# Kernel tuning notes

Hardware: AMD Instinct MI355X
Metric: run time of the kernel (lower is better)

Reference implementation:

```python
import jax, jax.numpy as jnp
import numpy as np

B, C, H, W = 4, 16, 256, 256
O = 32
KH = KW = 3
PAD = 1


def setup_inputs() -> dict:
    key = jax.random.key(0)
    ks = jax.random.split(key, 6)
    d_in = C * KH * KW          # 144
    d_out = O * KH * KW         # 288
    s1 = 1.0 / np.sqrt(d_in)
    s2 = 1.0 / np.sqrt(O)
    return {
        "x": jax.random.normal(ks[0], (B, C, H, W), dtype=jnp.float32),
        "W1": jax.random.uniform(ks[1], (O, d_in), jnp.float32, -s1, s1),
        "b1": jax.random.uniform(ks[2], (O,), jnp.float32, -s1, s1),
        "W2": jax.random.uniform(ks[3], (d_out, O), jnp.float32, -s2, s2),
        "b2": jax.random.uniform(ks[4], (d_out,), jnp.float32, -s2, s2),
        "bias": jax.random.uniform(ks[5], (O,), jnp.float32, -s1, s1),
    }


def _unfold(x):
    """im2col matching torch F.unfold ordering (c, kh, kw): -> [B, H*W, C*KH*KW]."""
    b, c, h, w = x.shape
    xp = jnp.pad(x, ((0, 0), (0, 0), (PAD, PAD), (PAD, PAD)))
    # stack the KH*KW shifted views: [B, C, KH*KW, H, W]
    shifts = [xp[:, :, i:i + h, j:j + w] for i in range(KH) for j in range(KW)]
    p = jnp.stack(shifts, axis=2)
    # -> [B, H, W, C, KH*KW] -> [B, L, C*KH*KW]  (c-major, then (i,j))
    p = p.transpose(0, 3, 4, 1, 2)
    return p.reshape(b, h * w, c * KH * KW)


def reference(x, W1, b1, W2, b2, bias):
    b, c, h, w = x.shape
    L = h * w
    feat = _unfold(x)                                   # [B, L, C*9]
    # per-pixel kernel generator MLP
    hid = jnp.tanh(jnp.einsum('blf,of->blo', feat, W1) + b1)          # [B, L, O]
    kern = jnp.einsum('blo,go->blg', hid, W2) + b2                    # [B, L, O*9]
    kern = kern.reshape(b, L, O, KH * KW)                             # [B, L, O, 9]
    # contract per-pixel kernel with its patch (channels summed):
    # out[b,l,o] = sum_{c,i,j} K[b,l,o,ij] * P[b,l,c,ij]
    patch_c = feat.reshape(b, L, c, KH * KW).sum(axis=2)              # [B, L, 9]
    out = jnp.einsum('blok,blk->blo', kern, patch_c)                  # [B, L, O]
    out = out.transpose(0, 2, 1).reshape(b, O, h, w)
    return out + bias[None, :, None, None]
```

## Files before the change

### kernel.cpp

```cpp
#include <hip/hip_runtime.h>

#define CC 16
#define OO 32
#define LL 65536

typedef __attribute__((ext_vector_type(8))) short bf16x8;
typedef __attribute__((ext_vector_type(4))) float f32x4;
typedef __attribute__((ext_vector_type(4))) int   i32x4;

static __device__ __forceinline__ ushort f2b(float f) {
    union { float f; unsigned u; } v; v.f = f;
    return (ushort)((v.u + 0x7fff + ((v.u >> 16) & 1)) >> 16);
}
static __device__ __forceinline__ unsigned pk2(float fl, float fh) {
    unsigned ul = __float_as_uint(fl) + 0x8000u;
    unsigned uh = __float_as_uint(fh) + 0x8000u;
    return __builtin_amdgcn_perm(uh, ul, 0x07060302);
}

__global__ void prepass(const float* __restrict__ W1, const float* __restrict__ b1,
                        const float* __restrict__ W2, const float* __restrict__ b2,
                        const float* __restrict__ bias,
                        ushort* __restrict__ w1f, ushort* __restrict__ w2f) {
    int idx = blockIdx.x * 256 + threadIdx.x;
    if (idx < 5120) {
        int f = idx >> 9, lane = (idx >> 3) & 63, j = idx & 7;
        int ks = f >> 1, ot = f & 1, lm = lane & 15, g = lane >> 4;
        int o = ot * 16 + lm, kk = ks * 32 + g * 8 + j;
        int r = kk >> 4, c = kk & 15;
        float v = (kk < 144) ? W1[o * 144 + c * 9 + r] : (kk == 144 ? b1[o] : 0.f);
        w1f[idx] = f2b(v);
    } else if (idx < 15360) {
        int i2 = idx - 5120;
        int f = i2 >> 9, lane = (i2 >> 3) & 63, j = i2 & 7;
        int ks = f >> 1, ot = f & 1, lm = lane & 15, g = lane >> 4;
        int o = ot * 16 + lm, kk = ks * 32 + g * 8 + j;
        float v;
        if      (kk < 288) v = W2[o * 288 + kk];
        else if (kk < 297) v = b2[o * 9 + (kk - 288)];
        else if (kk == 297) v = bias[o];
        else               v = 0.f;
        w2f[i2] = f2b(v);
    }
}

__global__ __launch_bounds__(256, 2) void dynaconv_mfma(
    const float* __restrict__ x, const ushort* __restrict__ w1f,
    const ushort* __restrict__ w2f, float* __restrict__ out)
{
    __shared__ __align__(16) ushort xs[4][260][24];
    __shared__ __align__(16) float  S[4][260];
    __shared__ __align__(16) float  hidT[4][16][36];

    const int tid  = threadIdx.x;
    const int wv   = tid >> 6;
    const int lane = tid & 63;
    const int g    = lane >> 4;
    const int lm   = lane & 15;

    const int vbid = (blockIdx.x & 7) * 64 + (blockIdx.x >> 3);
    const int b    = vbid >> 7;
    const int h0   = (vbid & 127) * 2;

    bf16x8 W1R[10], W2R[20];
#pragma unroll
    for (int f = 0; f < 10; ++f) W1R[f] = *(const bf16x8*)(w1f + (f * 64 + lane) * 8);
#pragma unroll
    for (int f = 0; f < 20; ++f) W2R[f] = *(const bf16x8*)(w2f + (f * 64 + lane) * 8);

    const float* xb = x + b * (CC * LL);
    {
        int offr[4]; bool okr[4];
#pragma unroll
        for (int r = 0; r < 4; ++r) {
            const int hh = h0 - 1 + r;
            okr[r] = (unsigned)hh < 256u;
            offr[r] = (okr[r] ? hh : 0) * 256 + tid;
        }
        float sr[4] = {0.f, 0.f, 0.f, 0.f};
#pragma unroll
        for (int cp = 0; cp < 8; ++cp) {
            const float* p0 = xb + (2 * cp) * LL;
            const float* p1 = p0 + LL;
#pragma unroll
            for (int r = 0; r < 4; ++r) {
                float va = p0[offr[r]], vb = p1[offr[r]];
                va = okr[r] ? va : 0.f; vb = okr[r] ? vb : 0.f;
                sr[r] += va + vb;
                *(unsigned*)&xs[r][tid + 1][2 * cp] = pk2(va, vb);
            }
        }
#pragma unroll
        for (int r = 0; r < 4; ++r) S[r][tid + 1] = sr[r];
        if (tid < 128) { int r = tid >> 5, side = (tid >> 4) & 1, c = tid & 15; xs[r][side * 257][c] = 0; }
        if (tid < 8)   S[tid >> 1][(tid & 1) * 257] = 0.f;
    }
    __syncthreads();

    int soff[5];
#pragma unroll
    for (int ks = 0; ks < 5; ++ks) {
        int r = 2 * ks + (g >> 1); if (r > 8) r = 8;
        int r3 = (r * 11) >> 5, rm = r - 3 * r3;
        soff[ks] = (r3 * 260 + rm + lm) * 24 + (g & 1) * 8;
    }
    const ushort* xsf = &xs[0][0][0];

    for (int hr = 0; hr < 2; ++hr) {
        const int hb = hr * (260 * 24);
#pragma unroll
        for (int t = 0; t < 4; ++t) {
            const int w0t = wv * 64 + t * 16;
            const int tb = w0t * 24 + hb;

            f32x4 a1[2] = {{0.f,0.f,0.f,0.f},{0.f,0.f,0.f,0.f}};
#pragma unroll
            for (int ks = 0; ks < 5; ++ks) {
                bf16x8 ff = *(const bf16x8*)(xsf + soff[ks] + tb);
                if (ks == 4) {
                    i32x4 wd = *(i32x4*)&ff;
                    wd[0] = (g < 2) ? wd[0] : (g == 2 ? 0x3F80 : 0);
                    wd[1] = (g < 2) ? wd[1] : 0;
                    wd[2] = (g < 2) ? wd[2] : 0;
                    wd[3] = (g < 2) ? wd[3] : 0;
                    ff = *(bf16x8*)&wd;
                }
                a1[0] = __builtin_amdgcn_mfma_f32_16x16x32_bf16(W1R[2 * ks],     ff, a1[0], 0, 0, 0);
                a1[1] = __builtin_amdgcn_mfma_f32_16x16x32_bf16(W1R[2 * ks + 1], ff, a1[1], 0, 0, 0);
            }

#pragma unroll
            for (int ot = 0; ot < 2; ++ot)
#pragma unroll
                for (int q = 0; q < 4; ++q) {
                    float e = __expf(2.f * a1[ot][q]);
                    hidT[wv][lm][ot * 16 + g * 4 + q] = 1.f - 2.f / (e + 1.f);
                }
            f32x4 h0v = *(const f32x4*)&hidT[wv][lm][g * 8];
            f32x4 h1v = *(const f32x4*)&hidT[wv][lm][g * 8 + 4];

            float pcv[9];
#pragma unroll
            for (int r = 0; r < 9; ++r) pcv[r] = S[r / 3 + hr][w0t + lm + (r % 3)];

            f32x4 a2[2] = {{0.f,0.f,0.f,0.f},{0.f,0.f,0.f,0.f}};
#pragma unroll
            for (int ks = 0; ks < 9; ++ks) {
                const float p = pcv[ks];
                i32x4 wd;
                wd[0] = (int)pk2(h0v[0] * p, h0v[1] * p);
                wd[1] = (int)pk2(h0v[2] * p, h0v[3] * p);
                wd[2] = (int)pk2(h1v[0] * p, h1v[1] * p);
                wd[3] = (int)pk2(h1v[2] * p, h1v[3] * p);
                bf16x8 ff2 = *(bf16x8*)&wd;
                a2[0] = __builtin_amdgcn_mfma_f32_16x16x32_bf16(W2R[2 * ks],     ff2, a2[0], 0, 0, 0);
                a2[1] = __builtin_amdgcn_mfma_f32_16x16x32_bf16(W2R[2 * ks + 1], ff2, a2[1], 0, 0, 0);
            }
            {
                i32x4 wd;
                wd[0] = (g == 0) ? (int)pk2(pcv[0], pcv[1]) : ((g == 1) ? (int)pk2(pcv[8], 1.f) : 0);
                wd[1] = (g == 0) ? (int)pk2(pcv[2], pcv[3]) : 0;
                wd[2] = (g == 0) ? (int)pk2(pcv[4], pcv[5]) : 0;
                wd[3] = (g == 0) ? (int)pk2(pcv[6], pcv[7]) : 0;
                bf16x8 ff2 = *(bf16x8*)&wd;
                a2[0] = __builtin_amdgcn_mfma_f32_16x16x32_bf16(W2R[18], ff2, a2[0], 0, 0, 0);
                a2[1] = __builtin_amdgcn_mfma_f32_16x16x32_bf16(W2R[19], ff2, a2[1], 0, 0, 0);
            }

            float* ob = out + b * (OO * LL) + (h0 + hr) * 256 + w0t + lm;
#pragma unroll
            for (int ot = 0; ot < 2; ++ot)
#pragma unroll
                for (int q = 0; q < 4; ++q)
                    __builtin_nontemporal_store(a2[ot][q], &ob[(ot * 16 + g * 4 + q) * LL]);
        }
    }
}

extern "C" void kernel_launch(void* const* d_in, const int* in_sizes, int n_in,
                              void* d_out, int out_size, void* d_ws, size_t ws_size,
                              hipStream_t stream) {
    const float* x    = (const float*)d_in[0];
    const float* W1   = (const float*)d_in[1];
    const float* b1   = (const float*)d_in[2];
    const float* W2   = (const float*)d_in[3];
    const float* b2   = (const float*)d_in[4];
    const float* bias = (const float*)d_in[5];
    float* out = (float*)d_out;

    ushort* w1f = (ushort*)d_ws;
    ushort* w2f = w1f + 5120;

    prepass<<<60, 256, 0, stream>>>(W1, b1, W2, b2, bias, w1f, w2f);
    dynaconv_mfma<<<512, 256, 0, stream>>>(x, w1f, w2f, out);
}
```

Before: 26.83 us.

## Use 512-thread blocks, stage W2 in LDS, and replace hidT LDS transpose with shuffles

Doubles the block to 512 threads, so each wave handles one output row and two 16-pixel tiles per iteration. W2 fragments move from registers into shared memory to lower register pressure for higher occupancy. The LDS round-trip used to transpose hidden activations is replaced by packed bf16 cross-lane shuffles. The x tile is shrunk to 16 channels with no padding, and the bias-one column now comes from a small LDS buffer. Output stores become regular rather than nontemporal. The costs are added LDS traffic for W2 on every MFMA and possible bank conflicts from the unpadded layout.

```diff
diff --git a/kernel.cpp b/kernel.cpp
--- a/kernel.cpp
+++ b/kernel.cpp
@@ -16,6 +16,10 @@
     unsigned ul = __float_as_uint(fl) + 0x8000u;
     unsigned uh = __float_as_uint(fh) + 0x8000u;
     return __builtin_amdgcn_perm(uh, ul, 0x07060302);
+}
+static __device__ __forceinline__ float tanh_fast(float x) {
+    float e = __expf(2.f * x);
+    return 1.f - 2.f / (e + 1.f);
 }
 
 __global__ void prepass(const float* __restrict__ W1, const float* __restrict__ b1,
@@ -44,13 +48,14 @@
     }
 }
 
-__global__ __launch_bounds__(256, 2) void dynaconv_mfma(
+__global__ __launch_bounds__(512, 4) void dynaconv_mfma(
     const float* __restrict__ x, const ushort* __restrict__ w1f,
     const ushort* __restrict__ w2f, float* __restrict__ out)
 {
-    __shared__ __align__(16) ushort xs[4][260][24];
-    __shared__ __align__(16) float  S[4][260];
-    __shared__ __align__(16) float  hidT[4][16][36];
+    __shared__ __align__(16) ushort xs[4][258][16];
+    __shared__ __align__(16) float  S[4][258];
+    __shared__ __align__(16) ushort extb[16];
+    __shared__ __align__(16) ushort W2L[20 * 512];
 
     const int tid  = threadIdx.x;
     const int wv   = tid >> 6;
@@ -62,39 +67,50 @@
     const int b    = vbid >> 7;
     const int h0   = (vbid & 127) * 2;
 
-    bf16x8 W1R[10], W2R[20];
+    bf16x8 W1R[10];
 #pragma unroll
     for (int f = 0; f < 10; ++f) W1R[f] = *(const bf16x8*)(w1f + (f * 64 + lane) * 8);
-#pragma unroll
-    for (int f = 0; f < 20; ++f) W2R[f] = *(const bf16x8*)(w2f + (f * 64 + lane) * 8);
+
+    {
+        const i32x4* src = (const i32x4*)w2f;
+        i32x4*       dst = (i32x4*)W2L;
+#pragma unroll
+        for (int k = 0; k < 3; ++k) {
+            int i = tid + k * 512;
+            if (i < 1280) dst[i] = src[i];
+        }
+    }
 
     const float* xb = x + b * (CC * LL);
     {
-        int offr[4]; bool okr[4];
-#pragma unroll
-        for (int r = 0; r < 4; ++r) {
-            const int hh = h0 - 1 + r;
-            okr[r] = (unsigned)hh < 256u;
-            offr[r] = (okr[r] ? hh : 0) * 256 + tid;
-        }
-        float sr[4] = {0.f, 0.f, 0.f, 0.f};
+        const int col = tid & 255;
+        const int rp  = tid >> 8;
+        const int ra  = rp * 2;
+        const int ha  = h0 - 1 + ra;
+        const int hbb = ha + 1;
+        const bool oka = (unsigned)ha  < 256u;
+        const bool okb = (unsigned)hbb < 256u;
+        const int offa = (oka ? ha  : 0) * 256 + col;
+        const int offb = (okb ? hbb : 0) * 256 + col;
+        float sa = 0.f, sb = 0.f;
 #pragma unroll
         for (int cp = 0; cp < 8; ++cp) {
             const float* p0 = xb + (2 * cp) * LL;
             const float* p1 = p0 + LL;
-#pragma unroll
-            for (int r = 0; r < 4; ++r) {
-                float va = p0[offr[r]], vb = p1[offr[r]];
-                va = okr[r] ? va : 0.f; vb = okr[r] ? vb : 0.f;
-                sr[r] += va + vb;
-                *(unsigned*)&xs[r][tid + 1][2 * cp] = pk2(va, vb);
-            }
-        }
-#pragma unroll
-        for (int r = 0; r < 4; ++r) S[r][tid + 1] = sr[r];
-        if (tid < 128) { int r = tid >> 5, side = (tid >> 4) & 1, c = tid & 15; xs[r][side * 257][c] = 0; }
-        if (tid < 8)   S[tid >> 1][(tid & 1) * 257] = 0.f;
-    }
+            float va0 = p0[offa], vb0 = p1[offa];
+            float va1 = p0[offb], vb1 = p1[offb];
+            va0 = oka ? va0 : 0.f; vb0 = oka ? vb0 : 0.f;
+            va1 = okb ? va1 : 0.f; vb1 = okb ? vb1 : 0.f;
+            sa += va0 + vb0; sb += va1 + vb1;
+            *(unsigned*)&xs[ra][col + 1][2 * cp]     = pk2(va0, vb0);
+            *(unsigned*)&xs[ra + 1][col + 1][2 * cp] = pk2(va1, vb1);
+        }
+        S[ra][col + 1] = sa; S[ra + 1][col + 1] = sb;
+    }
+    if (tid < 64) { int r = tid >> 4, side = (tid >> 3) & 1, cw = tid & 7;
+                    *(unsigned*)&xs[r][side * 257][2 * cw] = 0u; }
+    if (tid < 8)  S[tid >> 1][(tid & 1) * 257] = 0.f;
+    if (tid < 16) extb[tid] = (tid == 0) ? (ushort)0x3F80 : (ushort)0;
     __syncthreads();
 
     int soff[5];
@@ -102,77 +118,121 @@
     for (int ks = 0; ks < 5; ++ks) {
         int r = 2 * ks + (g >> 1); if (r > 8) r = 8;
         int r3 = (r * 11) >> 5, rm = r - 3 * r3;
-        soff[ks] = (r3 * 260 + rm + lm) * 24 + (g & 1) * 8;
+        soff[ks] = (r3 * 258 + rm + lm) * 16 + (g & 1) * 8;
     }
     const ushort* xsf = &xs[0][0][0];
-
-    for (int hr = 0; hr < 2; ++hr) {
-        const int hb = hr * (260 * 24);
-#pragma unroll
-        for (int t = 0; t < 4; ++t) {
-            const int w0t = wv * 64 + t * 16;
-            const int tb = w0t * 24 + hb;
-
-            f32x4 a1[2] = {{0.f,0.f,0.f,0.f},{0.f,0.f,0.f,0.f}};
-#pragma unroll
-            for (int ks = 0; ks < 5; ++ks) {
-                bf16x8 ff = *(const bf16x8*)(xsf + soff[ks] + tb);
-                if (ks == 4) {
-                    i32x4 wd = *(i32x4*)&ff;
-                    wd[0] = (g < 2) ? wd[0] : (g == 2 ? 0x3F80 : 0);
-                    wd[1] = (g < 2) ? wd[1] : 0;
-                    wd[2] = (g < 2) ? wd[2] : 0;
-                    wd[3] = (g < 2) ? wd[3] : 0;
-                    ff = *(bf16x8*)&wd;
-                }
-                a1[0] = __builtin_amdgcn_mfma_f32_16x16x32_bf16(W1R[2 * ks],     ff, a1[0], 0, 0, 0);
-                a1[1] = __builtin_amdgcn_mfma_f32_16x16x32_bf16(W1R[2 * ks + 1], ff, a1[1], 0, 0, 0);
-            }
-
-#pragma unroll
-            for (int ot = 0; ot < 2; ++ot)
-#pragma unroll
-                for (int q = 0; q < 4; ++q) {
-                    float e = __expf(2.f * a1[ot][q]);
-                    hidT[wv][lm][ot * 16 + g * 4 + q] = 1.f - 2.f / (e + 1.f);
-                }
-            f32x4 h0v = *(const f32x4*)&hidT[wv][lm][g * 8];
-            f32x4 h1v = *(const f32x4*)&hidT[wv][lm][g * 8 + 4];
-
-            float pcv[9];
-#pragma unroll
-            for (int r = 0; r < 9; ++r) pcv[r] = S[r / 3 + hr][w0t + lm + (r % 3)];
-
-            f32x4 a2[2] = {{0.f,0.f,0.f,0.f},{0.f,0.f,0.f,0.f}};
-#pragma unroll
-            for (int ks = 0; ks < 9; ++ks) {
-                const float p = pcv[ks];
-                i32x4 wd;
-                wd[0] = (int)pk2(h0v[0] * p, h0v[1] * p);
-                wd[1] = (int)pk2(h0v[2] * p, h0v[3] * p);
-                wd[2] = (int)pk2(h1v[0] * p, h1v[1] * p);
-                wd[3] = (int)pk2(h1v[2] * p, h1v[3] * p);
-                bf16x8 ff2 = *(bf16x8*)&wd;
-                a2[0] = __builtin_amdgcn_mfma_f32_16x16x32_bf16(W2R[2 * ks],     ff2, a2[0], 0, 0, 0);
-                a2[1] = __builtin_amdgcn_mfma_f32_16x16x32_bf16(W2R[2 * ks + 1], ff2, a2[1], 0, 0, 0);
-            }
-            {
-                i32x4 wd;
-                wd[0] = (g == 0) ? (int)pk2(pcv[0], pcv[1]) : ((g == 1) ? (int)pk2(pcv[8], 1.f) : 0);
-                wd[1] = (g == 0) ? (int)pk2(pcv[2], pcv[3]) : 0;
-                wd[2] = (g == 0) ? (int)pk2(pcv[4], pcv[5]) : 0;
-                wd[3] = (g == 0) ? (int)pk2(pcv[6], pcv[7]) : 0;
-                bf16x8 ff2 = *(bf16x8*)&wd;
-                a2[0] = __builtin_amdgcn_mfma_f32_16x16x32_bf16(W2R[18], ff2, a2[0], 0, 0, 0);
-                a2[1] = __builtin_amdgcn_mfma_f32_16x16x32_bf16(W2R[19], ff2, a2[1], 0, 0, 0);
-            }
-
-            float* ob = out + b * (OO * LL) + (h0 + hr) * 256 + w0t + lm;
-#pragma unroll
-            for (int ot = 0; ot < 2; ++ot)
-#pragma unroll
-                for (int q = 0; q < 4; ++q)
-                    __builtin_nontemporal_store(a2[ot][q], &ob[(ot * 16 + g * 4 + q) * LL]);
+    const ushort* w2b = W2L + lane * 8;
+    const int sA = ((g & 1) << 5) | lm;
+    const int sB = sA + 16;
+    const int hh = g >> 1;
+
+    const int hr = wv >> 2;
+    const int q  = wv & 3;
+
+#pragma unroll 1
+    for (int p = 0; p < 2; ++p) {
+        const int w0A = q * 64 + p * 32;
+        const int w0B = w0A + 16;
+        const int tbA = (hr * 258 + w0A) * 16;
+        const int tbB = tbA + 256;
+        const ushort* p4A = (g < 2) ? (xsf + soff[4] + tbA) : (extb + (g - 2) * 8);
+        const ushort* p4B = (g < 2) ? (xsf + soff[4] + tbB) : (extb + (g - 2) * 8);
+
+        f32x4 a1A0 = {0,0,0,0}, a1A1 = {0,0,0,0}, a1B0 = {0,0,0,0}, a1B1 = {0,0,0,0};
+#pragma unroll
+        for (int ks = 0; ks < 4; ++ks) {
+            bf16x8 fA = *(const bf16x8*)(xsf + soff[ks] + tbA);
+            bf16x8 fB = *(const bf16x8*)(xsf + soff[ks] + tbB);
+            a1A0 = __builtin_amdgcn_mfma_f32_16x16x32_bf16(W1R[2 * ks],     fA, a1A0, 0, 0, 0);
+            a1A1 = __builtin_amdgcn_mfma_f32_16x16x32_bf16(W1R[2 * ks + 1], fA, a1A1, 0, 0, 0);
+            a1B0 = __builtin_amdgcn_mfma_f32_16x16x32_bf16(W1R[2 * ks],     fB, a1B0, 0, 0, 0);
+            a1B1 = __builtin_amdgcn_mfma_f32_16x16x32_bf16(W1R[2 * ks + 1], fB, a1B1, 0, 0, 0);
+        }
+        {
+            bf16x8 fA = *(const bf16x8*)p4A;
+            bf16x8 fB = *(const bf16x8*)p4B;
+            a1A0 = __builtin_amdgcn_mfma_f32_16x16x32_bf16(W1R[8], fA, a1A0, 0, 0, 0);
+            a1A1 = __builtin_amdgcn_mfma_f32_16x16x32_bf16(W1R[9], fA, a1A1, 0, 0, 0);
+            a1B0 = __builtin_amdgcn_mfma_f32_16x16x32_bf16(W1R[8], fB, a1B0, 0, 0, 0);
+            a1B1 = __builtin_amdgcn_mfma_f32_16x16x32_bf16(W1R[9], fB, a1B1, 0, 0, 0);
+        }
+
+        unsigned WqA[4], WqB[4];
+#pragma unroll
+        for (int qq = 0; qq < 4; ++qq) {
+            WqA[qq] = pk2(tanh_fast(a1A0[qq]), tanh_fast(a1A1[qq]));
+            WqB[qq] = pk2(tanh_fast(a1B0[qq]), tanh_fast(a1B1[qq]));
+        }
+        float hfA[8], hfB[8];
+#pragma unroll
+        for (int qq = 0; qq < 4; ++qq) {
+            unsigned pa = (unsigned)__shfl((int)WqA[qq], sA);
+            unsigned pb = (unsigned)__shfl((int)WqA[qq], sB);
+            hfA[qq]     = __uint_as_float(hh ? (pa & 0xffff0000u) : (pa << 16));
+            hfA[4 + qq] = __uint_as_float(hh ? (pb & 0xffff0000u) : (pb << 16));
+            unsigned pc_ = (unsigned)__shfl((int)WqB[qq], sA);
+            unsigned pd  = (unsigned)__shfl((int)WqB[qq], sB);
+            hfB[qq]     = __uint_as_float(hh ? (pc_ & 0xffff0000u) : (pc_ << 16));
+            hfB[4 + qq] = __uint_as_float(hh ? (pd & 0xffff0000u) : (pd << 16));
+        }
+
+        float pcA[9], pcB[9];
+#pragma unroll
+        for (int r = 0; r < 9; ++r) {
+            pcA[r] = S[r / 3 + hr][w0A + lm + (r % 3)];
+            pcB[r] = S[r / 3 + hr][w0B + lm + (r % 3)];
+        }
+
+        f32x4 a2A0 = {0,0,0,0}, a2A1 = {0,0,0,0}, a2B0 = {0,0,0,0}, a2B1 = {0,0,0,0};
+#pragma unroll
+        for (int ks = 0; ks < 9; ++ks) {
+            bf16x8 bm0 = *(const bf16x8*)(w2b + (2 * ks) * 512);
+            bf16x8 bm1 = *(const bf16x8*)(w2b + (2 * ks + 1) * 512);
+            const float pA = pcA[ks], pB = pcB[ks];
+            i32x4 wA, wB;
+            wA[0] = (int)pk2(hfA[0] * pA, hfA[1] * pA);
+            wA[1] = (int)pk2(hfA[2] * pA, hfA[3] * pA);
+            wA[2] = (int)pk2(hfA[4] * pA, hfA[5] * pA);
+            wA[3] = (int)pk2(hfA[6] * pA, hfA[7] * pA);
+            wB[0] = (int)pk2(hfB[0] * pB, hfB[1] * pB);
+            wB[1] = (int)pk2(hfB[2] * pB, hfB[3] * pB);
+            wB[2] = (int)pk2(hfB[4] * pB, hfB[5] * pB);
+            wB[3] = (int)pk2(hfB[6] * pB, hfB[7] * pB);
+            bf16x8 fA = *(bf16x8*)&wA;
+            bf16x8 fB = *(bf16x8*)&wB;
+            a2A0 = __builtin_amdgcn_mfma_f32_16x16x32_bf16(bm0, fA, a2A0, 0, 0, 0);
+            a2A1 = __builtin_amdgcn_mfma_f32_16x16x32_bf16(bm1, fA, a2A1, 0, 0, 0);
+            a2B0 = __builtin_amdgcn_mfma_f32_16x16x32_bf16(bm0, fB, a2B0, 0, 0, 0);
+            a2B1 = __builtin_amdgcn_mfma_f32_16x16x32_bf16(bm1, fB, a2B1, 0, 0, 0);
+        }
+        {
+            bf16x8 bm0 = *(const bf16x8*)(w2b + 18 * 512);
+            bf16x8 bm1 = *(const bf16x8*)(w2b + 19 * 512);
+            i32x4 wA, wB;
+            wA[0] = (g == 0) ? (int)pk2(pcA[0], pcA[1]) : ((g == 1) ? (int)pk2(pcA[8], 1.f) : 0);
+            wA[1] = (g == 0) ? (int)pk2(pcA[2], pcA[3]) : 0;
+            wA[2] = (g == 0) ? (int)pk2(pcA[4], pcA[5]) : 0;
+            wA[3] = (g == 0) ? (int)pk2(pcA[6], pcA[7]) : 0;
+            wB[0] = (g == 0) ? (int)pk2(pcB[0], pcB[1]) : ((g == 1) ? (int)pk2(pcB[8], 1.f) : 0);
+            wB[1] = (g == 0) ? (int)pk2(pcB[2], pcB[3]) : 0;
+            wB[2] = (g == 0) ? (int)pk2(pcB[4], pcB[5]) : 0;
+            wB[3] = (g == 0) ? (int)pk2(pcB[6], pcB[7]) : 0;
+            bf16x8 fA = *(bf16x8*)&wA;
+            bf16x8 fB = *(bf16x8*)&wB;
+            a2A0 = __builtin_amdgcn_mfma_f32_16x16x32_bf16(bm0, fA, a2A0, 0, 0, 0);
+            a2A1 = __builtin_amdgcn_mfma_f32_16x16x32_bf16(bm1, fA, a2A1, 0, 0, 0);
+            a2B0 = __builtin_amdgcn_mfma_f32_16x16x32_bf16(bm0, fB, a2B0, 0, 0, 0);
+            a2B1 = __builtin_amdgcn_mfma_f32_16x16x32_bf16(bm1, fB, a2B1, 0, 0, 0);
+        }
+
+        float* obA = out + b * (OO * LL) + (h0 + hr) * 256 + w0A + lm;
+        float* obB = obA + 16;
+#pragma unroll
+        for (int qq = 0; qq < 4; ++qq) {
+            obA[(g * 4 + qq) * LL]        = a2A0[qq];
+            obA[(16 + g * 4 + qq) * LL]   = a2A1[qq];
+            obB[(g * 4 + qq) * LL]        = a2B0[qq];
+            obB[(16 + g * 4 + qq) * LL]   = a2B1[qq];
         }
     }
 }
@@ -192,5 +252,5 @@
     ushort* w2f = w1f + 5120;
 
     prepass<<<60, 256, 0, stream>>>(W1, b1, W2, b2, bias, w1f, w2f);
-    dynaconv_mfma<<<512, 256, 0, stream>>>(x, w1f, w2f, out);
-}
+    dynaconv_mfma<<<512, 512, 0, stream>>>(x, w1f, w2f, out);
+}
```

New measurement: 58.79 us. +119.1%, slower.
